# Kernel tuning notes

Hardware: AMD Instinct MI355X
Metric: run time of the kernel (lower is better)

Reference implementation:

```python
import jax, jax.numpy as jnp
import numpy as np
from jax import lax

L = 125  # lstm hidden size


def lstm_scan(xs, Wih, Whh, b):
    """PyTorch-LSTMCell math over a sequence. xs: [T, Din] -> hs: [T, L]."""
    def step(carry, x):
        h, c = carry
        g = x @ Wih.T + h @ Whh.T + b            # [4L]
        i, f, gg, o = jnp.split(g, 4)
        i = jax.nn.sigmoid(i)
        f = jax.nn.sigmoid(f)
        gg = jnp.tanh(gg)
        o = jax.nn.sigmoid(o)
        c = f * c + i * gg
        h = o * jnp.tanh(c)
        return (h, c), h
    h0 = jnp.zeros((L,), xs.dtype)
    c0 = jnp.zeros((L,), xs.dtype)
    _, hs = lax.scan(step, (h0, c0), xs)
    return hs


def bilstm(xs, Wih_f, Whh_f, b_f, Wih_b, Whh_b, b_b):
    hf = lstm_scan(xs, Wih_f, Whh_f, b_f)                 # forward hidden per token
    hb = lstm_scan(xs[::-1], Wih_b, Whh_b, b_b)[::-1]     # backward hidden per token
    # entry.lstms = [backward, forward]; cat order is [back, fwd]
    return jnp.concatenate([hb, hf], axis=-1)             # [T, 2L]


def setup_inputs() -> dict:
    key = jax.random.key(0)
    ks = jax.random.split(key, 20)
    T, V, P, WD, PD, H = 1024, 30003, 48, 100, 25, 100
    s = 0.1
    inp = {
        'word_ids': jax.random.randint(ks[0], (T,), 0, V),
        'pos_ids': jax.random.randint(ks[1], (T,), 0, P),
        'W_emb': jax.random.normal(ks[2], (V, WD), jnp.float32) * s,
        'P_emb': jax.random.normal(ks[3], (P, PD), jnp.float32) * s,
        'Wih_f0': jax.random.normal(ks[4], (4 * L, WD + PD), jnp.float32) * s,
        'Whh_f0': jax.random.normal(ks[5], (4 * L, L), jnp.float32) * s,
        'b_f0': jax.random.normal(ks[6], (4 * L,), jnp.float32) * s,
        'Wih_b0': jax.random.normal(ks[7], (4 * L, WD + PD), jnp.float32) * s,
        'Whh_b0': jax.random.normal(ks[8], (4 * L, L), jnp.float32) * s,
        'b_b0': jax.random.normal(ks[9], (4 * L,), jnp.float32) * s,
        'Wih_f1': jax.random.normal(ks[10], (4 * L, 2 * L), jnp.float32) * s,
        'Whh_f1': jax.random.normal(ks[11], (4 * L, L), jnp.float32) * s,
        'b_f1': jax.random.normal(ks[12], (4 * L,), jnp.float32) * s,
        'Wih_b1': jax.random.normal(ks[13], (4 * L, 2 * L), jnp.float32) * s,
        'Whh_b1': jax.random.normal(ks[14], (4 * L, L), jnp.float32) * s,
        'b_b1': jax.random.normal(ks[15], (4 * L,), jnp.float32) * s,
        'hidLayerFOH': jax.random.normal(ks[16], (2 * L, H), jnp.float32) * s,
        'hidLayerFOM': jax.random.normal(ks[17], (2 * L, H), jnp.float32) * s,
        'hidBias': jax.random.normal(ks[18], (H,), jnp.float32) * s,
        'outLayer': jax.random.normal(ks[19], (H, 1), jnp.float32) * s,
    }
    return inp


def reference(word_ids, pos_ids, W_emb, P_emb,
              Wih_f0, Whh_f0, b_f0, Wih_b0, Whh_b0, b_b0,
              Wih_f1, Whh_f1, b_f1, Wih_b1, Whh_b1, b_b1,
              hidLayerFOH, hidLayerFOM, hidBias, outLayer):
    # embedding concat: [T, wdims+pdims]
    x = jnp.concatenate([W_emb[word_ids], P_emb[pos_ids]], axis=-1)
    # first BiLSTM
    h1 = bilstm(x, Wih_f0, Whh_f0, b_f0, Wih_b0, Whh_b0, b_b0)     # [T, 2L]
    # second BiLSTM (bibiFlag)
    h2 = bilstm(h1, Wih_f1, Whh_f1, b_f1, Wih_b1, Whh_b1, b_b1)    # [T, 2L]
    # arc scorer over all (head i, modifier j) pairs
    head = h2 @ hidLayerFOH                                        # [T, H]
    mod = h2 @ hidLayerFOM                                         # [T, H]
    pair = jnp.tanh(head[:, None, :] + mod[None, :, :] + hidBias)  # [T, T, H]
    scores = (pair @ outLayer)[..., 0]                             # [T, T]
    return scores
```

## Files before the change

### kernel.cpp

```cpp
#include <hip/hip_runtime.h>
#include <math.h>

#define T_SEQ 1024
#define LH 125
#define G4 500

typedef _Float16 v8h __attribute__((ext_vector_type(8)));
typedef float f32x4 __attribute__((ext_vector_type(4)));

__device__ __forceinline__ float fsig(float x) {
    return __builtin_amdgcn_rcpf(1.f + __builtin_amdgcn_exp2f(x * -1.4426950408889634f));
}
__device__ __forceinline__ float ftanh(float x) {
    float e = __builtin_amdgcn_exp2f(x * -2.8853900817779268f);
    return 2.f * __builtin_amdgcn_rcpf(1.f + e) - 1.f;
}

__device__ __forceinline__ v8h packa8(const float* __restrict__ rowp, int kbase) {
    v8h r;
#define PA(j) { int k = kbase + (j); r[j] = (k < LH) ? (_Float16)rowp[k] : (_Float16)0.f; }
    PA(0) PA(1) PA(2) PA(3) PA(4) PA(5) PA(6) PA(7)
#undef PA
    return r;
}

__global__ void k_preproj0(const int* __restrict__ wid, const int* __restrict__ pid,
                           const float* __restrict__ W_emb, const float* __restrict__ P_emb,
                           const float* __restrict__ Wf, const float* __restrict__ bf,
                           const float* __restrict__ Wb, const float* __restrict__ bb,
                           float* __restrict__ pf, float* __restrict__ pb) {
    __shared__ float xs[8][128];
    const int t0 = blockIdx.x * 8;
    const int tid = threadIdx.x;
    for (int tt = 0; tt < 8; ++tt) {
        int t = t0 + tt;
        for (int k = tid; k < 125; k += 512)
            xs[tt][k] = (k < 100) ? W_emb[wid[t] * 100 + k] : P_emb[pid[t] * 25 + (k - 100)];
    }
    __syncthreads();
    const int j = tid;
    if (j < G4) {
        const float* wf = Wf + j * 125;
        const float* wb = Wb + j * 125;
        float af[8], ab[8];
        float bfv = bf[j], bbv = bb[j];
        #pragma unroll
        for (int tt = 0; tt < 8; ++tt) { af[tt] = bfv; ab[tt] = bbv; }
        #pragma unroll 5
        for (int k = 0; k < 125; ++k) {
            float wfk = wf[k], wbk = wb[k];
            #pragma unroll
            for (int tt = 0; tt < 8; ++tt) {
                float xv = xs[tt][k];
                af[tt] += wfk * xv;
                ab[tt] += wbk * xv;
            }
        }
        int g = j / 125, u = j - g * 125;
        int off = u * 4 + g;
        #pragma unroll
        for (int tt = 0; tt < 8; ++tt) {
            pf[(t0 + tt) * G4 + off] = af[tt];
            pb[(t0 + tt) * G4 + off] = ab[tt];
        }
    }
}

__global__ void k_preproj1(const float* __restrict__ h1,
                           const float* __restrict__ Wf, const float* __restrict__ bf,
                           const float* __restrict__ Wb, const float* __restrict__ bb,
                           float* __restrict__ pf, float* __restrict__ pb) {
    __shared__ float xs[8][256];
    const int t0 = blockIdx.x * 8;
    const int tid = threadIdx.x;
    for (int tt = 0; tt < 8; ++tt) {
        int t = t0 + tt;
        for (int k = tid; k < 250; k += 512) xs[tt][k] = h1[t * 250 + k];
    }
    __syncthreads();
    const int j = tid;
    if (j < G4) {
        const float* wf = Wf + j * 250;
        const float* wb = Wb + j * 250;
        float af[8], ab[8];
        float bfv = bf[j], bbv = bb[j];
        #pragma unroll
        for (int tt = 0; tt < 8; ++tt) { af[tt] = bfv; ab[tt] = bbv; }
        #pragma unroll 2
        for (int k = 0; k < 250; ++k) {
            float wfk = wf[k], wbk = wb[k];
            #pragma unroll
            for (int tt = 0; tt < 8; ++tt) {
                float xv = xs[tt][k];
                af[tt] += wfk * xv;
                ab[tt] += wbk * xv;
            }
        }
        int g = j / 125, u = j - g * 125;
        int off = u * 4 + g;
        #pragma unroll
        for (int tt = 0; tt < 8; ++tt) {
            pf[(t0 + tt) * G4 + off] = af[tt];
            pb[(t0 + tt) * G4 + off] = ab[tt];
        }
    }
}

__global__ void __attribute__((amdgpu_flat_work_group_size(512, 512)))
__attribute__((amdgpu_waves_per_eu(2, 2)))
k_scan(const float* __restrict__ pf, const float* __restrict__ Wf,
       const float* __restrict__ pb, const float* __restrict__ Wb,
       float* __restrict__ hout) {
    const int dir = blockIdx.x;
    const float* __restrict__ pre = dir ? pb : pf;
    const float* __restrict__ Whh = dir ? Wb : Wf;
    const int col0 = dir ? 0 : 125;

    __shared__ __align__(32) _Float16 h_lds[2 * 128];

    const int t9   = threadIdx.x;
    const int w    = t9 >> 6;
    const int lane = t9 & 63;
    const int lane15 = lane & 15;
    const int hi16   = lane >> 4;
    const bool mb0 = (lane & 1) != 0;
    const bool mb1 = (lane & 2) != 0;

    const int uo    = 4 * (lane & 3) + hi16;
    const int u_raw = 16 * w + uo;
    const bool valid = (u_raw < LH);
    const int u = valid ? u_raw : (LH - 1);
    const bool writer = ((lane & 12) == 0) && valid;

#define LROW(m) int ro##m; { int rp = 64 * w + 16 * m + lane15; if (rp > 499) rp = 499; \
                             ro##m = (rp & 3) * 125 + (rp >> 2); }
    LROW(0) LROW(1) LROW(2) LROW(3)
#undef LROW
#define LA(m) v8h a##m##0 = packa8(Whh + ro##m * LH, hi16 * 8); \
              v8h a##m##1 = packa8(Whh + ro##m * LH, 32 + hi16 * 8); \
              v8h a##m##2 = packa8(Whh + ro##m * LH, 64 + hi16 * 8); \
              v8h a##m##3 = packa8(Whh + ro##m * LH, 96 + hi16 * 8);
    LA(0) LA(1) LA(2) LA(3)
#undef LA

    for (int q = t9; q < 2 * 128; q += 512) h_lds[q] = (_Float16)0.f;
    float c = 0.f;
    __syncthreads();

    const int pstride = dir ? -G4 : G4;
    int poff = (dir ? (T_SEQ - 1) * G4 : 0) + u * 4;
    const int gstride = dir ? -250 : 250;
    int goff = (dir ? (T_SEQ - 1) * 250 : 0) + col0 + u;
    float4 pv4 = *reinterpret_cast<const float4*>(pre + poff);
    poff += pstride;

    const int bbase = hi16 * 8;

#define SCAN_STEP(CUR, NXT) { \
    float4 pvn = *reinterpret_cast<const float4*>(pre + poff); poff += pstride; \
    const _Float16* hb = &h_lds[(CUR) * 128 + bbase]; \
    v8h bb0 = *reinterpret_cast<const v8h*>(hb); \
    v8h bb1 = *reinterpret_cast<const v8h*>(hb + 32); \
    v8h bb2 = *reinterpret_cast<const v8h*>(hb + 64); \
    v8h bb3 = *reinterpret_cast<const v8h*>(hb + 96); \
    f32x4 z = {0.f, 0.f, 0.f, 0.f}; \
    f32x4 acc0 = __builtin_amdgcn_mfma_f32_16x16x32_f16(a00, bb0, z, 0, 0, 0); \
    acc0 = __builtin_amdgcn_mfma_f32_16x16x32_f16(a01, bb1, acc0, 0, 0, 0); \
    acc0 = __builtin_amdgcn_mfma_f32_16x16x32_f16(a02, bb2, acc0, 0, 0, 0); \
    acc0 = __builtin_amdgcn_mfma_f32_16x16x32_f16(a03, bb3, acc0, 0, 0, 0); \
    f32x4 acc1 = __builtin_amdgcn_mfma_f32_16x16x32_f16(a10, bb0, z, 0, 0, 0); \
    acc1 = __builtin_amdgcn_mfma_f32_16x16x32_f16(a11, bb1, acc1, 0, 0, 0); \
    acc1 = __builtin_amdgcn_mfma_f32_16x16x32_f16(a12, bb2, acc1, 0, 0, 0); \
    acc1 = __builtin_amdgcn_mfma_f32_16x16x32_f16(a13, bb3, acc1, 0, 0, 0); \
    f32x4 acc2 = __builtin_amdgcn_mfma_f32_16x16x32_f16(a20, bb0, z, 0, 0, 0); \
    acc2 = __builtin_amdgcn_mfma_f32_16x16x32_f16(a21, bb1, acc2, 0, 0, 0); \
    acc2 = __builtin_amdgcn_mfma_f32_16x16x32_f16(a22, bb2, acc2, 0, 0, 0); \
    acc2 = __builtin_amdgcn_mfma_f32_16x16x32_f16(a23, bb3, acc2, 0, 0, 0); \
    f32x4 acc3 = __builtin_amdgcn_mfma_f32_16x16x32_f16(a30, bb0, z, 0, 0, 0); \
    acc3 = __builtin_amdgcn_mfma_f32_16x16x32_f16(a31, bb1, acc3, 0, 0, 0); \
    acc3 = __builtin_amdgcn_mfma_f32_16x16x32_f16(a32, bb2, acc3, 0, 0, 0); \
    acc3 = __builtin_amdgcn_mfma_f32_16x16x32_f16(a33, bb3, acc3, 0, 0, 0); \
    float x01_0 = mb0 ? acc1[0] : acc0[0]; float x23_0 = mb0 ? acc3[0] : acc2[0]; \
    float x01_1 = mb0 ? acc1[1] : acc0[1]; float x23_1 = mb0 ? acc3[1] : acc2[1]; \
    float x01_2 = mb0 ? acc1[2] : acc0[2]; float x23_2 = mb0 ? acc3[2] : acc2[2]; \
    float x01_3 = mb0 ? acc1[3] : acc0[3]; float x23_3 = mb0 ? acc3[3] : acc2[3]; \
    float fr0 = mb1 ? x23_0 : x01_0; \
    float fr1 = mb1 ? x23_1 : x01_1; \
    float fr2 = mb1 ? x23_2 : x01_2; \
    float fr3 = mb1 ? x23_3 : x01_3; \
    float gi = fsig(fr0 + pv4.x); \
    float gf = fsig(fr1 + pv4.y); \
    float gg = ftanh(fr2 + pv4.z); \
    float go = fsig(fr3 + pv4.w); \
    c = gf * c + gi * gg; \
    float hnew = go * ftanh(c); \
    if (writer) { \
        h_lds[(NXT) * 128 + u] = (_Float16)hnew; \
        hout[goff] = hnew; \
    } \
    goff += gstride; \
    __syncthreads(); \
    pv4 = pvn; \
}

    for (int s2 = 0; s2 < T_SEQ; s2 += 2) {
        SCAN_STEP(0, 1)
        SCAN_STEP(1, 0)
    }
#undef SCAN_STEP
}

__global__ void k_headmod(const float* __restrict__ h2,
                          const float* __restrict__ FOH, const float* __restrict__ FOM,
                          const float* __restrict__ bias,
                          float* __restrict__ headp, float* __restrict__ modv) {
    __shared__ float hs[250];
    int t = blockIdx.x, tid = threadIdx.x;
    for (int k = tid; k < 250; k += 256) hs[k] = h2[t * 250 + k];
    __syncthreads();
    if (tid < 100) {
        float a = 0.f;
        #pragma unroll 5
        for (int k = 0; k < 250; ++k) a += hs[k] * FOH[k * 100 + tid];
        headp[t * 100 + tid] = a + bias[tid];
    } else if (tid >= 128 && tid < 228) {
        int h = tid - 128;
        float a = 0.f;
        #pragma unroll 5
        for (int k = 0; k < 250; ++k) a += hs[k] * FOM[k * 100 + h];
        modv[t * 100 + h] = a;
    }
}

__global__ void k_score(const float* __restrict__ headp, const float* __restrict__ modv,
                        const float* __restrict__ outw, float* __restrict__ out) {
    __shared__ float hh[32][100];
    __shared__ float mm[32][100];
    __shared__ float ow[100];
    const int bi = blockIdx.y, bj = blockIdx.x;
    const int tx = threadIdx.x, ty = threadIdx.y;
    const int tid = ty * 16 + tx;
    for (int q = tid; q < 3200; q += 256) {
        int r = q / 100, cidx = q % 100;
        hh[r][cidx] = headp[(bi * 32 + r) * 100 + cidx];
        mm[r][cidx] = modv[(bj * 32 + r) * 100 + cidx];
    }
    if (tid < 100) ow[tid] = outw[tid];
    __syncthreads();
    float a00 = 0.f, a01 = 0.f, a10 = 0.f, a11 = 0.f;
    #pragma unroll 5
    for (int h = 0; h < 100; h += 4) {
        float4 ha = *reinterpret_cast<const float4*>(&hh[ty][h]);
        float4 hb = *reinterpret_cast<const float4*>(&hh[ty + 16][h]);
        float4 ma = *reinterpret_cast<const float4*>(&mm[tx][h]);
        float4 mb = *reinterpret_cast<const float4*>(&mm[tx + 16][h]);
        float4 wv = *reinterpret_cast<const float4*>(&ow[h]);
#define SC(J, HA, HB, MA, MB, WV) { \
        a00 += ftanh(HA + MA) * WV; \
        a01 += ftanh(HA + MB) * WV; \
        a10 += ftanh(HB + MA) * WV; \
        a11 += ftanh(HB + MB) * WV; }
        SC(0, ha.x, hb.x, ma.x, mb.x, wv.x)
        SC(1, ha.y, hb.y, ma.y, mb.y, wv.y)
        SC(2, ha.z, hb.z, ma.z, mb.z, wv.z)
        SC(3, ha.w, hb.w, ma.w, mb.w, wv.w)
#undef SC
    }
    const int r0 = bi * 32 + ty, c0g = bj * 32 + tx;
    out[r0 * 1024 + c0g]               = a00;
    out[r0 * 1024 + c0g + 16]          = a01;
    out[(r0 + 16) * 1024 + c0g]        = a10;
    out[(r0 + 16) * 1024 + c0g + 16]   = a11;
}

extern "C" void kernel_launch(void* const* d_in, const int* in_sizes, int n_in,
                              void* d_out, int out_size, void* d_ws, size_t ws_size,
                              hipStream_t stream) {
    const int*   wid    = (const int*)d_in[0];
    const int*   pid    = (const int*)d_in[1];
    const float* W_emb  = (const float*)d_in[2];
    const float* P_emb  = (const float*)d_in[3];
    const float* Wih_f0 = (const float*)d_in[4];
    const float* Whh_f0 = (const float*)d_in[5];
    const float* b_f0   = (const float*)d_in[6];
    const float* Wih_b0 = (const float*)d_in[7];
    const float* Whh_b0 = (const float*)d_in[8];
    const float* b_b0   = (const float*)d_in[9];
    const float* Wih_f1 = (const float*)d_in[10];
    const float* Whh_f1 = (const float*)d_in[11];
    const float* b_f1   = (const float*)d_in[12];
    const float* Wih_b1 = (const float*)d_in[13];
    const float* Whh_b1 = (const float*)d_in[14];
    const float* b_b1   = (const float*)d_in[15];
    const float* FOH    = (const float*)d_in[16];
    const float* FOM    = (const float*)d_in[17];
    const float* hidB   = (const float*)d_in[18];
    const float* outW   = (const float*)d_in[19];
    float* out = (float*)d_out;
    float* ws  = (float*)d_ws;

    float* pf    = ws;
    float* pb    = pf    + 512000;
    float* h1    = pb    + 512000;
    float* h2    = h1    + 256000;
    float* headp = h2    + 256000;
    float* modv  = headp + 102400;

    k_preproj0<<<128, 512, 0, stream>>>(wid, pid, W_emb, P_emb,
                                        Wih_f0, b_f0, Wih_b0, b_b0, pf, pb);
    k_scan<<<2, 512, 0, stream>>>(pf, Whh_f0, pb, Whh_b0, h1);

    k_preproj1<<<128, 512, 0, stream>>>(h1, Wih_f1, b_f1, Wih_b1, b_b1, pf, pb);
    k_scan<<<2, 512, 0, stream>>>(pf, Whh_f1, pb, Whh_b1, h2);

    k_headmod<<<T_SEQ, 256, 0, stream>>>(h2, FOH, FOM, hidB, headp, modv);
    dim3 gs(32, 32), bs(16, 16);
    k_score<<<gs, bs, 0, stream>>>(headp, modv, outW, out);
}
```

Before: 1.031 ms.

## Halve scan workgroup to 4 waves with 8 MFMA row-tiles per wave

```diff
diff --git a/kernel.cpp b/kernel.cpp
--- a/kernel.cpp
+++ b/kernel.cpp
@@ -106,8 +106,8 @@
     }
 }
 
-__global__ void __attribute__((amdgpu_flat_work_group_size(512, 512)))
-__attribute__((amdgpu_waves_per_eu(2, 2)))
+__global__ void __attribute__((amdgpu_flat_work_group_size(256, 256)))
+__attribute__((amdgpu_waves_per_eu(1, 1)))
 k_scan(const float* __restrict__ pf, const float* __restrict__ Wf,
        const float* __restrict__ pb, const float* __restrict__ Wb,
        float* __restrict__ hout) {
@@ -123,27 +123,28 @@
     const int lane = t9 & 63;
     const int lane15 = lane & 15;
     const int hi16   = lane >> 4;
-    const bool mb0 = (lane & 1) != 0;
-    const bool mb1 = (lane & 2) != 0;
-
-    const int uo    = 4 * (lane & 3) + hi16;
-    const int u_raw = 16 * w + uo;
+    const bool b0 = (lane & 1) != 0;
+    const bool b1 = (lane & 2) != 0;
+    const bool b2 = (lane & 4) != 0;
+
+    const int msel  = lane & 7;
+    const int u_raw = 32 * w + 4 * msel + hi16;
     const bool valid = (u_raw < LH);
     const int u = valid ? u_raw : (LH - 1);
-    const bool writer = ((lane & 12) == 0) && valid;
-
-#define LROW(m) int ro##m; { int rp = 64 * w + 16 * m + lane15; if (rp > 499) rp = 499; \
+    const bool writer = ((lane & 8) == 0) && valid;
+
+#define LROW(m) int ro##m; { int rp = 128 * w + 16 * m + lane15; if (rp > 499) rp = 499; \
                              ro##m = (rp & 3) * 125 + (rp >> 2); }
-    LROW(0) LROW(1) LROW(2) LROW(3)
+    LROW(0) LROW(1) LROW(2) LROW(3) LROW(4) LROW(5) LROW(6) LROW(7)
 #undef LROW
 #define LA(m) v8h a##m##0 = packa8(Whh + ro##m * LH, hi16 * 8); \
               v8h a##m##1 = packa8(Whh + ro##m * LH, 32 + hi16 * 8); \
               v8h a##m##2 = packa8(Whh + ro##m * LH, 64 + hi16 * 8); \
               v8h a##m##3 = packa8(Whh + ro##m * LH, 96 + hi16 * 8);
-    LA(0) LA(1) LA(2) LA(3)
+    LA(0) LA(1) LA(2) LA(3) LA(4) LA(5) LA(6) LA(7)
 #undef LA
 
-    for (int q = t9; q < 2 * 128; q += 512) h_lds[q] = (_Float16)0.f;
+    for (int q = t9; q < 2 * 128; q += 256) h_lds[q] = (_Float16)0.f;
     float c = 0.f;
     __syncthreads();
 
@@ -155,6 +156,22 @@
     poff += pstride;
 
     const int bbase = hi16 * 8;
+
+#define MM(m) \
+    f32x4 acc##m = __builtin_amdgcn_mfma_f32_16x16x32_f16(a##m##0, bb0, z, 0, 0, 0); \
+    acc##m = __builtin_amdgcn_mfma_f32_16x16x32_f16(a##m##1, bb1, acc##m, 0, 0, 0); \
+    acc##m = __builtin_amdgcn_mfma_f32_16x16x32_f16(a##m##2, bb2, acc##m, 0, 0, 0); \
+    acc##m = __builtin_amdgcn_mfma_f32_16x16x32_f16(a##m##3, bb3, acc##m, 0, 0, 0);
+
+#define MSEL(r) \
+    float fr##r; { \
+        float s01 = b0 ? acc1[r] : acc0[r]; \
+        float s23 = b0 ? acc3[r] : acc2[r]; \
+        float s45 = b0 ? acc5[r] : acc4[r]; \
+        float s67 = b0 ? acc7[r] : acc6[r]; \
+        float t0s = b1 ? s23 : s01; \
+        float t1s = b1 ? s67 : s45; \
+        fr##r = b2 ? t1s : t0s; }
 
 #define SCAN_STEP(CUR, NXT) { \
     float4 pvn = *reinterpret_cast<const float4*>(pre + poff); poff += pstride; \
@@ -164,30 +181,8 @@
     v8h bb2 = *reinterpret_cast<const v8h*>(hb + 64); \
     v8h bb3 = *reinterpret_cast<const v8h*>(hb + 96); \
     f32x4 z = {0.f, 0.f, 0.f, 0.f}; \
-    f32x4 acc0 = __builtin_amdgcn_mfma_f32_16x16x32_f16(a00, bb0, z, 0, 0, 0); \
-    acc0 = __builtin_amdgcn_mfma_f32_16x16x32_f16(a01, bb1, acc0, 0, 0, 0); \
-    acc0 = __builtin_amdgcn_mfma_f32_16x16x32_f16(a02, bb2, acc0, 0, 0, 0); \
-    acc0 = __builtin_amdgcn_mfma_f32_16x16x32_f16(a03, bb3, acc0, 0, 0, 0); \
-    f32x4 acc1 = __builtin_amdgcn_mfma_f32_16x16x32_f16(a10, bb0, z, 0, 0, 0); \
-    acc1 = __builtin_amdgcn_mfma_f32_16x16x32_f16(a11, bb1, acc1, 0, 0, 0); \
-    acc1 = __builtin_amdgcn_mfma_f32_16x16x32_f16(a12, bb2, acc1, 0, 0, 0); \
-    acc1 = __builtin_amdgcn_mfma_f32_16x16x32_f16(a13, bb3, acc1, 0, 0, 0); \
-    f32x4 acc2 = __builtin_amdgcn_mfma_f32_16x16x32_f16(a20, bb0, z, 0, 0, 0); \
-    acc2 = __builtin_amdgcn_mfma_f32_16x16x32_f16(a21, bb1, acc2, 0, 0, 0); \
-    acc2 = __builtin_amdgcn_mfma_f32_16x16x32_f16(a22, bb2, acc2, 0, 0, 0); \
-    acc2 = __builtin_amdgcn_mfma_f32_16x16x32_f16(a23, bb3, acc2, 0, 0, 0); \
-    f32x4 acc3 = __builtin_amdgcn_mfma_f32_16x16x32_f16(a30, bb0, z, 0, 0, 0); \
-    acc3 = __builtin_amdgcn_mfma_f32_16x16x32_f16(a31, bb1, acc3, 0, 0, 0); \
-    acc3 = __builtin_amdgcn_mfma_f32_16x16x32_f16(a32, bb2, acc3, 0, 0, 0); \
-    acc3 = __builtin_amdgcn_mfma_f32_16x16x32_f16(a33, bb3, acc3, 0, 0, 0); \
-    float x01_0 = mb0 ? acc1[0] : acc0[0]; float x23_0 = mb0 ? acc3[0] : acc2[0]; \
-    float x01_1 = mb0 ? acc1[1] : acc0[1]; float x23_1 = mb0 ? acc3[1] : acc2[1]; \
-    float x01_2 = mb0 ? acc1[2] : acc0[2]; float x23_2 = mb0 ? acc3[2] : acc2[2]; \
-    float x01_3 = mb0 ? acc1[3] : acc0[3]; float x23_3 = mb0 ? acc3[3] : acc2[3]; \
-    float fr0 = mb1 ? x23_0 : x01_0; \
-    float fr1 = mb1 ? x23_1 : x01_1; \
-    float fr2 = mb1 ? x23_2 : x01_2; \
-    float fr3 = mb1 ? x23_3 : x01_3; \
+    MM(0) MM(1) MM(2) MM(3) MM(4) MM(5) MM(6) MM(7) \
+    MSEL(0) MSEL(1) MSEL(2) MSEL(3) \
     float gi = fsig(fr0 + pv4.x); \
     float gf = fsig(fr1 + pv4.y); \
     float gg = ftanh(fr2 + pv4.z); \
@@ -208,6 +203,8 @@
         SCAN_STEP(1, 0)
     }
 #undef SCAN_STEP
+#undef MSEL
+#undef MM
 }
 
 __global__ void k_headmod(const float* __restrict__ h2,
@@ -255,15 +252,15 @@
         float4 ma = *reinterpret_cast<const float4*>(&mm[tx][h]);
         float4 mb = *reinterpret_cast<const float4*>(&mm[tx + 16][h]);
         float4 wv = *reinterpret_cast<const float4*>(&ow[h]);
-#define SC(J, HA, HB, MA, MB, WV) { \
+#define SC(HA, HB, MA, MB, WV) { \
         a00 += ftanh(HA + MA) * WV; \
         a01 += ftanh(HA + MB) * WV; \
         a10 += ftanh(HB + MA) * WV; \
         a11 += ftanh(HB + MB) * WV; }
-        SC(0, ha.x, hb.x, ma.x, mb.x, wv.x)
-        SC(1, ha.y, hb.y, ma.y, mb.y, wv.y)
-        SC(2, ha.z, hb.z, ma.z, mb.z, wv.z)
-        SC(3, ha.w, hb.w, ma.w, mb.w, wv.w)
+        SC(ha.x, hb.x, ma.x, mb.x, wv.x)
+        SC(ha.y, hb.y, ma.y, mb.y, wv.y)
+        SC(ha.z, hb.z, ma.z, mb.z, wv.z)
+        SC(ha.w, hb.w, ma.w, mb.w, wv.w)
 #undef SC
     }
     const int r0 = bi * 32 + ty, c0g = bj * 32 + tx;
@@ -308,10 +305,10 @@
 
     k_preproj0<<<128, 512, 0, stream>>>(wid, pid, W_emb, P_emb,
                                         Wih_f0, b_f0, Wih_b0, b_b0, pf, pb);
-    k_scan<<<2, 512, 0, stream>>>(pf, Whh_f0, pb, Whh_b0, h1);
+    k_scan<<<2, 256, 0, stream>>>(pf, Whh_f0, pb, Whh_b0, h1);
 
     k_preproj1<<<128, 512, 0, stream>>>(h1, Wih_f1, b_f1, Wih_b1, b_b1, pf, pb);
-    k_scan<<<2, 512, 0, stream>>>(pf, Whh_f1, pb, Whh_b1, h2);
+    k_scan<<<2, 256, 0, stream>>>(pf, Whh_f1, pb, Whh_b1, h2);
 
     k_headmod<<<T_SEQ, 256, 0, stream>>>(h2, FOH, FOM, hidB, headp, modv);
     dim3 gs(32, 32), bs(16, 16);
```

Result: slower. 1.237 ms (+20.0%).
